# Optimization experiments

Measured on AMD Instinct MI355X. Metric: run time of the kernel, lower is better.

Reference implementation:

```python
import jax, jax.numpy as jnp
import numpy as np

B_, S_, D_ = 2, 1024, 768
EXPAND, HEADDIM, DSTATE = 2, 64, 64
DINNER = EXPAND * D_            # 1536
NHEADS = DINNER // HEADDIM      # 24
DMLP = int(2.5 * D_)            # 1920
PROJ = 2 * DINNER + 2 * NHEADS * DSTATE + NHEADS + NHEADS * (DSTATE // 2)  # 6936


def rms_norm(x, w, eps=1e-5):
    return x * jax.lax.rsqrt(jnp.mean(x * x, axis=-1, keepdims=True) + eps) * w


def apply_rope(x, angles):
    # x: (..., d_state), angles: (..., d_state//2)
    x1 = x[..., 0::2]
    x2 = x[..., 1::2]
    c, s = jnp.cos(angles), jnp.sin(angles)
    even = c * x1 - s * x2
    odd = s * x1 + c * x2
    return jnp.stack([even, odd], axis=-1).reshape(x.shape)


def ssm_scan(x, A, Bm, Cm):
    # x: (b,s,h,p), A: (b,s,h), Bm/Cm: (b,s,h,n)
    b, s, h, p = x.shape
    n = Bm.shape[-1]

    def step(hstate, inp):
        x_t, A_t, B_t, C_t = inp
        hstate = hstate * jnp.exp(A_t)[:, :, None, None] + jnp.einsum('bhn,bhp->bhpn', B_t, x_t)
        y_t = jnp.einsum('bhpn,bhn->bhp', hstate, C_t)
        return hstate, y_t

    h0 = jnp.zeros((b, h, p, n), dtype=x.dtype)
    xs = (jnp.swapaxes(x, 0, 1), jnp.swapaxes(A, 0, 1),
          jnp.swapaxes(Bm, 0, 1), jnp.swapaxes(Cm, 0, 1))
    _, ys = jax.lax.scan(step, h0, xs)
    return jnp.swapaxes(ys, 0, 1)  # (b,s,h,p)


def setup_inputs() -> dict:
    key = jax.random.key(0)
    ks = jax.random.split(key, 16)
    sc = 0.02
    return {
        'x': jax.random.normal(ks[0], (B_, S_, D_), dtype=jnp.float32),
        'norm1_w': jnp.ones((D_,), jnp.float32),
        'norm2_w': jnp.ones((D_,), jnp.float32),
        'in_proj_w': jax.random.normal(ks[1], (PROJ, D_), jnp.float32) * sc,
        'out_proj_w': jax.random.normal(ks[2], (D_, DINNER), jnp.float32) * sc,
        'A_log': jax.random.uniform(ks[3], (NHEADS,), jnp.float32, -4.0, -1.0),
        'D': jnp.ones((NHEADS,), jnp.float32),
        'dt_bias': jax.random.uniform(ks[4], (NHEADS,), jnp.float32, 0.001, 0.1),
        'B_bias': jnp.ones((1, NHEADS, DSTATE), jnp.float32),
        'C_bias': jnp.ones((1, NHEADS, DSTATE), jnp.float32),
        'Bnorm_w': jnp.ones((DSTATE,), jnp.float32),
        'Cnorm_w': jnp.ones((DSTATE,), jnp.float32),
        'mlp_gate_w': jax.random.normal(ks[5], (DMLP, D_), jnp.float32) * sc,
        'mlp_up_w': jax.random.normal(ks[6], (DMLP, D_), jnp.float32) * sc,
        'mlp_down_w': jax.random.normal(ks[7], (D_, DMLP), jnp.float32) * sc,
    }


def reference(x, norm1_w, norm2_w, in_proj_w, out_proj_w, A_log, D, dt_bias,
              B_bias, C_bias, Bnorm_w, Cnorm_w, mlp_gate_w, mlp_up_w, mlp_down_w):
    b, s, _ = x.shape
    h = rms_norm(x, norm1_w)
    proj = jnp.einsum('bsd,od->bso', h, in_proj_w)
    i = 0
    z = proj[..., i:i + DINNER]; i += DINNER
    x_ssm = proj[..., i:i + DINNER]; i += DINNER
    Bm = proj[..., i:i + NHEADS * DSTATE].reshape(b, s, NHEADS, DSTATE); i += NHEADS * DSTATE
    Cm = proj[..., i:i + NHEADS * DSTATE].reshape(b, s, NHEADS, DSTATE); i += NHEADS * DSTATE
    dt = proj[..., i:i + NHEADS]; i += NHEADS
    theta = proj[..., i:].reshape(b, s, NHEADS, DSTATE // 2)

    dt = jax.nn.softplus(dt + dt_bias)                 # (b,s,h)
    A = -jnp.exp(A_log) * dt                           # (b,s,h)
    alpha = jnp.exp(A)
    gamma = (alpha - 1.0) / (A + 1e-6) * 0.5 + 1.0

    Bm = rms_norm(Bm, Bnorm_w) + B_bias
    Cm = rms_norm(Cm, Cnorm_w) + C_bias
    cum_theta = jnp.cumsum(dt[..., None] * theta, axis=1)
    Bm = apply_rope(Bm, cum_theta)
    Cm = apply_rope(Cm, cum_theta)

    x_ssm = x_ssm.reshape(b, s, NHEADS, HEADDIM)
    x_scaled = x_ssm * gamma[..., None]
    y = ssm_scan(x_scaled, A, Bm, Cm)                  # (b,s,h,p)
    skip = (D[None, None, :] * x_ssm.sum(-1))[..., None]  # (b,s,h,1)
    y = (y + skip).reshape(b, s, DINNER)
    y = y * (z * jax.nn.sigmoid(z))
    y = jnp.einsum('bsi,oi->bso', y, out_proj_w)
    x = x + y
    h2 = rms_norm(x, norm2_w)
    g = jnp.einsum('bsd,od->bso', h2, mlp_gate_w)
    u = jnp.einsum('bsd,od->bso', h2, mlp_up_w)
    mlp = jnp.einsum('bsi,oi->bso', (g * jax.nn.sigmoid(g)) * u, mlp_down_w)
    return x + mlp
```

## Files before the change

### kernel.cpp

```cpp
#include <hip/hip_runtime.h>

typedef unsigned short u16;
typedef __attribute__((ext_vector_type(8))) short short8;
typedef __attribute__((ext_vector_type(4))) float f32x4;

constexpr int B_N    = 2;
constexpr int SEQ    = 1024;
constexpr int DMODEL = 768;
constexpr int DINNER = 1536;
constexpr int NH     = 24;
constexpr int DMLP   = 1920;
constexpr int NPROJ  = 6936;
constexpr int PP     = 7040;
constexpr int MROWS  = B_N * SEQ;
constexpr int NCHUNK = 16;
constexpr int CLEN   = 64;

__device__ __forceinline__ u16 f2bf(float f) {
  union { float f; unsigned u; } x; x.f = f;
  unsigned r = x.u + 0x7fffu + ((x.u >> 16) & 1u);
  return (u16)(r >> 16);
}
__device__ __forceinline__ float bf2f(u16 b) {
  union { unsigned u; float f; } x; x.u = ((unsigned)b) << 16; return x.f;
}

__device__ __forceinline__ void gld_lds16(const u16* g, u16* l) {
  __builtin_amdgcn_global_load_lds((const __attribute__((address_space(1))) void*)g,
                                   (__attribute__((address_space(3))) void*)l, 16, 0, 0);
}

__device__ __forceinline__ short8 frag(const u16* base, int row, int cb) {
  return *(const short8*)(base + row * 64 + ((cb ^ (row & 7)) << 3));
}
__device__ __forceinline__ int swz_idx(int row, int e) {
  return (((e >> 3) ^ (row & 7)) << 3) | (e & 7);
}

constexpr size_t E0  = (size_t)PP * DMODEL;
constexpr size_t E0s = (size_t)NPROJ * DMODEL;
constexpr size_t E1  = (size_t)DMODEL * DINNER;
constexpr size_t E2  = (size_t)DMLP * DMODEL;
constexpr size_t ETOT = E0 + E1 + 3 * E2;

__global__ void cast_all_kernel(const float* __restrict__ w_in, const float* __restrict__ w_out,
                                const float* __restrict__ w_g, const float* __restrict__ w_u,
                                const float* __restrict__ w_d,
                                u16* __restrict__ wb_in, u16* __restrict__ wb_out,
                                u16* __restrict__ wb_gu, u16* __restrict__ wb_d) {
  size_t i = ((size_t)blockIdx.x * 256 + threadIdx.x) * 4;
  if (i >= ETOT) return;
  float4 v; u16* dst;
  if (i < E0) {
    dst = wb_in + i;
    if (i < E0s) v = *(const float4*)(w_in + i);
    else { v.x = v.y = v.z = v.w = 0.f; }
  } else if (i < E0 + E1) {
    size_t k = i - E0; dst = wb_out + k; v = *(const float4*)(w_out + k);
  } else if (i < E0 + E1 + 2 * E2) {
    size_t k = i - E0 - E1;
    size_t r = k / DMODEL, col = k - r * DMODEL;
    const float* src = (r & 1) ? w_u : w_g;
    v = *(const float4*)(src + (r >> 1) * DMODEL + col);
    dst = wb_gu + k;
  } else {
    size_t k = i - E0 - E1 - 2 * E2; dst = wb_d + k; v = *(const float4*)(w_d + k);
  }
  short4 o;
  o.x = (short)f2bf(v.x); o.y = (short)f2bf(v.y);
  o.z = (short)f2bf(v.z); o.w = (short)f2bf(v.w);
  *(short4*)dst = o;
}

__global__ __launch_bounds__(256) void add_rmsnorm_kernel(
    const float* __restrict__ a, const float* __restrict__ b,
    const float* __restrict__ w, float* __restrict__ sum_out,
    u16* __restrict__ hout) {
  int row = blockIdx.x;
  int t = threadIdx.x;
  const float* pa = a + (size_t)row * DMODEL;
  const float* pb = b ? b + (size_t)row * DMODEL : nullptr;
  float v[3]; float ss = 0.f;
#pragma unroll
  for (int i = 0; i < 3; ++i) {
    int c = t + i * 256;
    float x = pa[c];
    if (pb) x += pb[c];
    v[i] = x; ss += x * x;
  }
#pragma unroll
  for (int o = 32; o > 0; o >>= 1) ss += __shfl_xor(ss, o);
  __shared__ float red[4];
  if ((t & 63) == 0) red[t >> 6] = ss;
  __syncthreads();
  ss = red[0] + red[1] + red[2] + red[3];
  float sc = rsqrtf(ss * (1.f / DMODEL) + 1e-5f);
#pragma unroll
  for (int i = 0; i < 3; ++i) {
    int c = t + i * 256;
    if (sum_out) sum_out[(size_t)row * DMODEL + c] = v[i];
    hout[(size_t)row * DMODEL + c] = f2bf(v[i] * sc * w[c]);
  }
}

template<int BM, int BN, int MODE>
__global__ __launch_bounds__(256) void gemm_bt_kernel(
    const u16* __restrict__ A, const u16* __restrict__ Bw,
    void* __restrict__ Cv, int K, int ldc, const float* __restrict__ addsrc) {
  constexpr int MI = BM / 32;
  constexpr int NJ = BN / 32;
  __shared__ u16 As[BM * 64];
  __shared__ u16 Bs[BN * 64];
  const int t = threadIdx.x;
  const int lane = t & 63;
  const int wave = t >> 6;
  const int wm = wave >> 1, wn = wave & 1;
  const int gx = gridDim.x, gy = gridDim.y;
  const int o = blockIdx.y * gx + blockIdx.x;
  const int nwg = gx * gy;
  const int cid = (o & 7) * (nwg >> 3) + (o >> 3);
  const int bx = cid / gy, by = cid - bx * gy;
  const int m0 = by * BM, n0 = bx * BN;
  f32x4 acc[MI][NJ] = {};
  const int rr = t >> 3;
  const int kc = (t & 7) * 8;
  const u16* ga = A + (size_t)(m0 + rr) * K + kc;
  const u16* gb = Bw + (size_t)(n0 + rr) * K + kc;
  for (int kt = 0; kt < K; kt += 64) {
    __syncthreads();
#pragma unroll
    for (int i = 0; i < MI; ++i)
      gld_lds16(ga + (size_t)i * 32 * K + kt, As + i * 2048 + t * 8);
#pragma unroll
    for (int i = 0; i < NJ; ++i)
      gld_lds16(gb + (size_t)i * 32 * K + kt, Bs + i * 2048 + t * 8);
    __syncthreads();
#pragma unroll
    for (int kh = 0; kh < 2; ++kh) {
      short8 af[MI], bfr[NJ];
#pragma unroll
      for (int i = 0; i < MI; ++i)
        af[i] = *(const short8*)(As + (wm * (BM / 2) + i * 16 + (lane & 15)) * 64 + kh * 32 + (lane >> 4) * 8);
#pragma unroll
      for (int j = 0; j < NJ; ++j)
        bfr[j] = *(const short8*)(Bs + (wn * (BN / 2) + j * 16 + (lane & 15)) * 64 + kh * 32 + (lane >> 4) * 8);
#pragma unroll
      for (int i = 0; i < MI; ++i)
#pragma unroll
        for (int j = 0; j < NJ; ++j)
          acc[i][j] = __builtin_amdgcn_mfma_f32_16x16x32_bf16(af[i], bfr[j], acc[i][j], 0, 0, 0);
    }
  }
  const int cr = (lane >> 4) * 4;
  const int cc = lane & 15;
#pragma unroll
  for (int i = 0; i < MI; ++i) {
#pragma unroll
    for (int j = 0; j < NJ; ++j) {
      int row = m0 + wm * (BM / 2) + i * 16 + cr;
      int col = n0 + wn * (BN / 2) + j * 16 + cc;
      if (MODE == 0) {
        float* C = (float*)Cv;
        float* cp = C + (size_t)row * ldc + col;
        if (addsrc) {
          const float* ap = addsrc + (size_t)row * ldc + col;
#pragma unroll
          for (int r = 0; r < 4; ++r) cp[(size_t)r * ldc] = acc[i][j][r] + ap[(size_t)r * ldc];
        } else {
#pragma unroll
          for (int r = 0; r < 4; ++r) cp[(size_t)r * ldc] = acc[i][j][r];
        }
      } else if (MODE == 1) {
        u16* C = (u16*)Cv;
#pragma unroll
        for (int r = 0; r < 4; ++r)
          C[(size_t)(row + r) * ldc + col] = f2bf(acc[i][j][r]);
      } else {
        u16* C = (u16*)Cv;
#pragma unroll
        for (int r = 0; r < 4; ++r) {
          float v = acc[i][j][r];
          float p = __shfl_xor(v, 1);
          if ((lane & 1) == 0) {
            float g = v, u = p;
            float res = g / (1.f + __expf(-g)) * u;
            C[(size_t)(row + r) * ldc + (col >> 1)] = f2bf(res);
          }
        }
      }
    }
  }
}

__global__ __launch_bounds__(256) void prep_kernel(
    u16* __restrict__ proj, const float* __restrict__ A_log,
    const float* __restrict__ Dv, const float* __restrict__ dt_bias,
    const float* __restrict__ B_bias, const float* __restrict__ C_bias,
    const float* __restrict__ Bnw, const float* __restrict__ Cnw,
    float* __restrict__ Abuf, float* __restrict__ skip_b,
    float* __restrict__ dtheta) {
  int wid = blockIdx.x * 4 + (threadIdx.x >> 6);
  int lane = threadIdx.x & 63;
  int m = wid / NH, h = wid - m * NH;
  u16* row = proj + (size_t)m * PP;

  float Braw = bf2f(row[3072 + h * 64 + lane]);
  float Craw = bf2f(row[4608 + h * 64 + lane]);
  float sb = Braw * Braw, sc2 = Craw * Craw;
#pragma unroll
  for (int o = 32; o > 0; o >>= 1) { sb += __shfl_xor(sb, o); sc2 += __shfl_xor(sc2, o); }
  float rb = rsqrtf(sb * (1.f / 64.f) + 1e-5f);
  float rc = rsqrtf(sc2 * (1.f / 64.f) + 1e-5f);
  row[3072 + h * 64 + lane] = f2bf(Braw * rb * Bnw[lane] + B_bias[h * 64 + lane]);
  row[4608 + h * 64 + lane] = f2bf(Craw * rc * Cnw[lane] + C_bias[h * 64 + lane]);

  float dtr = bf2f(row[6144 + h]) + dt_bias[h];
  float dt = dtr > 20.f ? dtr : log1pf(__expf(dtr));
  float A = -__expf(A_log[h]) * dt;
  float alpha = __expf(A);
  float gamma = (alpha - 1.f) / (A + 1e-6f) * 0.5f + 1.f;

  float xv = bf2f(row[1536 + h * 64 + lane]);
  float sx = xv;
#pragma unroll
  for (int o = 32; o > 0; o >>= 1) sx += __shfl_xor(sx, o);
  row[1536 + h * 64 + lane] = f2bf(xv * gamma);

  if (lane == 0) {
    Abuf[(size_t)m * NH + h] = A;
    skip_b[(size_t)m * NH + h] = Dv[h] * sx;
  }
  if (lane < 32) {
    float th = bf2f(row[6168 + h * 32 + lane]);
    dtheta[(size_t)m * 768 + h * 32 + lane] = dt * th;
  }
}

__global__ __launch_bounds__(256) void cumsum_a_kernel(float* __restrict__ dtheta,
                                                       float* __restrict__ ctot) {
  int bid = blockIdx.x;
  int cb = bid % 3, rest = bid / 3;
  int c = rest & 15, b = rest >> 4;
  int col = cb * 256 + threadIdx.x;
  float* p = dtheta + ((size_t)(b * SEQ + c * CLEN)) * 768 + col;
  float acc = 0.f;
#pragma unroll 4
  for (int s = 0; s < CLEN; ++s) {
    acc += p[(size_t)s * 768];
    p[(size_t)s * 768] = acc;
  }
  ctot[((size_t)b * NCHUNK + c) * 768 + col] = acc;
}

__global__ void cumsum_b_kernel(float* __restrict__ ctot) {
  int tid = blockIdx.x * 256 + threadIdx.x;
  int b = tid / 768, col = tid - b * 768;
  float pre = 0.f;
#pragma unroll
  for (int c = 0; c < NCHUNK; ++c) {
    size_t o = ((size_t)b * NCHUNK + c) * 768 + col;
    float v = ctot[o];
    ctot[o] = pre;
    pre += v;
  }
}

__global__ __launch_bounds__(256) void rope_kernel(
    u16* __restrict__ proj, const float* __restrict__ dtheta,
    const float* __restrict__ ctot) {
  int wid = blockIdx.x * 4 + (threadIdx.x >> 6);
  int lane = threadIdx.x & 63;
  int m = wid / NH, h = wid - m * NH;
  int j = lane & 31;
  int b = m >> 10;
  int c = (m >> 6) & 15;
  float ang = dtheta[(size_t)m * 768 + h * 32 + j] +
              ctot[((size_t)b * NCHUNK + c) * 768 + h * 32 + j];
  float sn, cs;
  __sincosf(ang, &sn, &cs);
  int base = (lane < 32) ? 3072 : 4608;
  unsigned* p = (unsigned*)(proj + (size_t)m * PP + base + h * 64) + j;
  unsigned v = *p;
  float x1 = bf2f((u16)(v & 0xffffu));
  float x2 = bf2f((u16)(v >> 16));
  *p = (unsigned)f2bf(cs * x1 - sn * x2) | ((unsigned)f2bf(sn * x1 + cs * x2) << 16);
}

__global__ __launch_bounds__(256) void houtA_kernel(
    const u16* __restrict__ proj, const float* __restrict__ Abuf,
    float* __restrict__ Lbuf, float* __restrict__ Hbuf) {
  int c = blockIdx.x & 15, bh = blockIdx.x >> 4;
  int b = bh / NH, h = bh - b * NH;
  int t = threadIdx.x, w = t >> 6, l = t & 63;
  __shared__ float sTmp[64][65];
  __shared__ u16 sBT[64 * 64];
  __shared__ u16 sXT[64 * 64];
  __shared__ float sRatio[64];
  int m0 = b * SEQ + c * CLEN;
  if (w == 0) {
    float v = Abuf[(size_t)(m0 + l) * NH + h];
#pragma unroll
    for (int o = 1; o < 64; o <<= 1) {
      float u = __shfl_up(v, o);
      if (l >= o) v += u;
    }
    Lbuf[(size_t)(m0 + l) * NH + h] = v;
    float L63 = __shfl(v, 63);
    sRatio[l] = __expf(L63 - v);
  }
  int rr = t >> 2, q = t & 3;
  {
    const u16* row = proj + (size_t)(m0 + rr) * PP + 3072 + h * 64;
#pragma unroll
    for (int k = 0; k < 4; ++k) {
      int e = q * 16 + k * 4;
      short4 sv = *(const short4*)(row + e);
      float4 ov;
      ov.x = bf2f((u16)sv.x); ov.y = bf2f((u16)sv.y);
      ov.z = bf2f((u16)sv.z); ov.w = bf2f((u16)sv.w);
      *(float4*)&sTmp[rr][e] = ov;
    }
  }
  __syncthreads();
  {
#pragma unroll
    for (int k = 0; k < 8; ++k) {
      int tw = (l + w * 8 + k) & 31;
      int t0 = tw * 2;
      unsigned pk = (unsigned)f2bf(sTmp[t0][l]) | ((unsigned)f2bf(sTmp[t0 + 1][l]) << 16);
      *(unsigned*)(sBT + l * 64 + swz_idx(l, t0)) = pk;
    }
  }
  __syncthreads();
  {
    const u16* row = proj + (size_t)(m0 + rr) * PP + 1536 + h * 64;
#pragma unroll
    for (int k = 0; k < 4; ++k) {
      int e = q * 16 + k * 4;
      short4 sv = *(const short4*)(row + e);
      float4 ov;
      ov.x = bf2f((u16)sv.x); ov.y = bf2f((u16)sv.y);
      ov.z = bf2f((u16)sv.z); ov.w = bf2f((u16)sv.w);
      *(float4*)&sTmp[rr][e] = ov;
    }
  }
  __syncthreads();
  {
#pragma unroll
    for (int k = 0; k < 8; ++k) {
      int tw = (l + w * 8 + k) & 31;
      int t0 = tw * 2;
      float v0 = sTmp[t0][l] * sRatio[t0];
      float v1 = sTmp[t0 + 1][l] * sRatio[t0 + 1];
      unsigned pk = (unsigned)f2bf(v0) | ((unsigned)f2bf(v1) << 16);
      *(unsigned*)(sXT + l * 64 + swz_idx(l, t0)) = pk;
    }
  }
  __syncthreads();
  f32x4 acc[4] = {};
#pragma unroll
  for (int kh = 0; kh < 2; ++kh) {
    int cb = kh * 4 + (l >> 4);
    short8 af = frag(sXT, w * 16 + (l & 15), cb);
#pragma unroll
    for (int j = 0; j < 4; ++j)
      acc[j] = __builtin_amdgcn_mfma_f32_16x16x32_bf16(af, frag(sBT, j * 16 + (l & 15), cb), acc[j], 0, 0, 0);
  }
  float* Hp = Hbuf + ((size_t)(bh * NCHUNK + c)) * 4096;
  int pr = w * 16 + ((l >> 4) << 2);
#pragma unroll
  for (int j = 0; j < 4; ++j)
#pragma unroll
    for (int r = 0; r < 4; ++r)
      Hp[(size_t)(pr + r) * 64 + j * 16 + (l & 15)] = acc[j][r];
}

__global__ __launch_bounds__(256) void scan2_kernel(
    float* __restrict__ Hbuf, const float* __restrict__ Lbuf) {
  int bh = blockIdx.x >> 4;
  int e = (blockIdx.x & 15) * 256 + threadIdx.x;
  int b = bh / NH, h = bh - b * NH;
  float S = 0.f;
  for (int c = 0; c < NCHUNK; ++c) {
    float* Hp = Hbuf + ((size_t)(bh * NCHUNK + c)) * 4096 + e;
    float P = __expf(Lbuf[(size_t)(b * SEQ + c * CLEN + CLEN - 1) * NH + h]);
    float v = *Hp;
    *Hp = S;
    S = P * S + v;
  }
}

__global__ __launch_bounds__(256) void intraB_kernel(
    const u16* __restrict__ proj, const float* __restrict__ Hbuf,
    const float* __restrict__ Lbuf, const float* __restrict__ skip_b,
    u16* __restrict__ actb) {
  int c = blockIdx.x & 15, bh = blockIdx.x >> 4;
  int b = bh / NH, h = bh - b * NH;
  int t = threadIdx.x, w = t >> 6, l = t & 63;
  __shared__ u16 sC[64 * 64];
  __shared__ u16 sBH[64 * 64];
  __shared__ u16 sXT[64 * 64];
  __shared__ union UU { float tmp[64][65]; u16 gm[64 * 64]; } uS;
  __shared__ float sL[64], sSkip[64];
  int m0 = b * SEQ + c * CLEN;
  if (w == 0) {
    sL[l] = Lbuf[(size_t)(m0 + l) * NH + h];
    sSkip[l] = skip_b[(size_t)(m0 + l) * NH + h];
  }
  int rr = t >> 2, q = t & 3;
  {
    const u16* rowC = proj + (size_t)(m0 + rr) * PP + 4608 + h * 64;
    const u16* rowB = proj + (size_t)(m0 + rr) * PP + 3072 + h * 64;
    const u16* rowX = proj + (size_t)(m0 + rr) * PP + 1536 + h * 64;
#pragma unroll
    for (int k = 0; k < 4; ++k) {
      int e = q * 16 + k * 4;
      int idx = swz_idx(rr, e);
      short4 cv = *(const short4*)(rowC + e);
      *(unsigned*)(sC + rr * 64 + idx)     = (unsigned)(u16)cv.x | ((unsigned)(u16)cv.y << 16);
      *(unsigned*)(sC + rr * 64 + idx + 2) = (unsigned)(u16)cv.z | ((unsigned)(u16)cv.w << 16);
      short4 bv = *(const short4*)(rowB + e);
      *(unsigned*)(sBH + rr * 64 + idx)     = (unsigned)(u16)bv.x | ((unsigned)(u16)bv.y << 16);
      *(unsigned*)(sBH + rr * 64 + idx + 2) = (unsigned)(u16)bv.z | ((unsigned)(u16)bv.w << 16);
      short4 xv = *(const short4*)(rowX + e);
      float4 ov;
      ov.x = bf2f((u16)xv.x); ov.y = bf2f((u16)xv.y);
      ov.z = bf2f((u16)xv.z); ov.w = bf2f((u16)xv.w);
      *(float4*)&uS.tmp[rr][e] = ov;
    }
  }
  __syncthreads();
  {
#pragma unroll
    for (int k = 0; k < 8; ++k) {
      int tw = (l + w * 8 + k) & 31;
      int t0 = tw * 2;
      unsigned pk = (unsigned)f2bf(uS.tmp[t0][l]) | ((unsigned)f2bf(uS.tmp[t0 + 1][l]) << 16);
      *(unsigned*)(sXT + l * 64 + swz_idx(l, t0)) = pk;
    }
  }
  __syncthreads();
  f32x4 g4[4] = {};
#pragma unroll
  for (int kh = 0; kh < 2; ++kh) {
    int cb = kh * 4 + (l >> 4);
    short8 af = frag(sC, w * 16 + (l & 15), cb);
#pragma unroll
    for (int j = 0; j < 4; ++j)
      g4[j] = __builtin_amdgcn_mfma_f32_16x16x32_bf16(af, frag(sBH, j * 16 + (l & 15), cb), g4[j], 0, 0, 0);
  }
  __syncthreads();
  {
    int sr = w * 16 + ((l >> 4) << 2);
#pragma unroll
    for (int j = 0; j < 4; ++j) {
      int tc = j * 16 + (l & 15);
#pragma unroll
      for (int r = 0; r < 4; ++r) {
        int s = sr + r;
        float gv = (tc <= s) ? g4[j][r] * __expf(sL[s] - sL[tc]) : 0.f;
        uS.gm[s * 64 + swz_idx(s, tc)] = f2bf(gv);
      }
    }
    const float* Hp = Hbuf + ((size_t)(bh * NCHUNK + c)) * 4096 + rr * 64;
#pragma unroll
    for (int k = 0; k < 4; ++k) {
      int e = q * 16 + k * 4;
      float4 v = *(const float4*)(Hp + e);
      unsigned lo = (unsigned)f2bf(v.x) | ((unsigned)f2bf(v.y) << 16);
      unsigned hi = (unsigned)f2bf(v.z) | ((unsigned)f2bf(v.w) << 16);
      int idx = swz_idx(rr, e);
      *(unsigned*)(sBH + rr * 64 + idx) = lo;
      *(unsigned*)(sBH + rr * 64 + idx + 2) = hi;
    }
  }
  __syncthreads();
  f32x4 y1[4] = {}, y2[4] = {};
#pragma unroll
  for (int kh = 0; kh < 2; ++kh) {
    int cb = kh * 4 + (l >> 4);
    short8 ag = frag(uS.gm, w * 16 + (l & 15), cb);
    short8 ac = frag(sC, w * 16 + (l & 15), cb);
#pragma unroll
    for (int j = 0; j < 4; ++j) {
      y1[j] = __builtin_amdgcn_mfma_f32_16x16x32_bf16(ag, frag(sXT, j * 16 + (l & 15), cb), y1[j], 0, 0, 0);
      y2[j] = __builtin_amdgcn_mfma_f32_16x16x32_bf16(ac, frag(sBH, j * 16 + (l & 15), cb), y2[j], 0, 0, 0);
    }
  }
  int sr = w * 16 + ((l >> 4) << 2);
#pragma unroll
  for (int r = 0; r < 4; ++r) {
    int s = sr + r;
    float scale = __expf(sL[s]);
    float skp = sSkip[s];
    size_t mrow = (size_t)(m0 + s);
#pragma unroll
    for (int j = 0; j < 4; ++j) {
      int p = j * 16 + (l & 15);
      float y = y1[j][r] + scale * y2[j][r] + skp;
      float z = bf2f(proj[mrow * PP + h * 64 + p]);
      float sg = 1.f / (1.f + __expf(-z));
      actb[mrow * DINNER + h * 64 + p] = f2bf(y * z * sg);
    }
  }
}

extern "C" void kernel_launch(void* const* d_in, const int* in_sizes, int n_in,
                              void* d_out, int out_size, void* d_ws, size_t ws_size,
                              hipStream_t stream) {
  (void)in_sizes; (void)n_in; (void)out_size; (void)ws_size;
  const float* x      = (const float*)d_in[0];
  const float* n1w    = (const float*)d_in[1];
  const float* n2w    = (const float*)d_in[2];
  const float* w_in   = (const float*)d_in[3];
  const float* w_out  = (const float*)d_in[4];
  const float* A_log  = (const float*)d_in[5];
  const float* Dv     = (const float*)d_in[6];
  const float* dt_b   = (const float*)d_in[7];
  const float* B_bias = (const float*)d_in[8];
  const float* C_bias = (const float*)d_in[9];
  const float* Bnw    = (const float*)d_in[10];
  const float* Cnw    = (const float*)d_in[11];
  const float* w_g    = (const float*)d_in[12];
  const float* w_u    = (const float*)d_in[13];
  const float* w_d    = (const float*)d_in[14];
  float* out = (float*)d_out;

  char* ws = (char*)d_ws;
  size_t off = 0;
  auto alloc = [&](size_t bytes) -> char* {
    char* p = ws + off;
    off = (off + bytes + 255) & ~(size_t)255;
    return p;
  };
  u16*   wb_in  = (u16*)  alloc(E0 * 2);
  u16*   wb_out = (u16*)  alloc(E1 * 2);
  u16*   wb_gu  = (u16*)  alloc(E2 * 2 * 2);
  u16*   wb_d   = (u16*)  alloc(E2 * 2);
  u16*   h1     = (u16*)  alloc((size_t)MROWS * DMODEL * 2);
  u16*   proj   = (u16*)  alloc((size_t)MROWS * PP * 2);
  float* Abuf   = (float*)alloc((size_t)MROWS * NH * 4);
  float* skip_b = (float*)alloc((size_t)MROWS * NH * 4);
  float* Lbuf   = (float*)alloc((size_t)MROWS * NH * 4);
  float* dtheta = (float*)alloc((size_t)MROWS * 768 * 4);
  float* ctot   = (float*)alloc((size_t)B_N * NCHUNK * 768 * 4);
  float* Hbuf   = (float*)alloc((size_t)B_N * NH * NCHUNK * 4096 * 4);
  u16*   actb   = (u16*)  alloc((size_t)MROWS * DINNER * 2);
  float* tmp1   = (float*)alloc((size_t)MROWS * DMODEL * 4);
  float* x2     = (float*)alloc((size_t)MROWS * DMODEL * 4);
  u16*   h2     = (u16*)  alloc((size_t)MROWS * DMODEL * 2);
  u16*   gub    = (u16*)  alloc((size_t)MROWS * DMLP * 2);

  cast_all_kernel<<<(int)((ETOT / 4 + 255) / 256), 256, 0, stream>>>(
      w_in, w_out, w_g, w_u, w_d, wb_in, wb_out, wb_gu, wb_d);
  add_rmsnorm_kernel<<<MROWS, 256, 0, stream>>>(x, nullptr, n1w, nullptr, h1);
  {
    dim3 g(PP / 128, MROWS / 64);
    gemm_bt_kernel<64, 128, 1><<<g, 256, 0, stream>>>(h1, wb_in, proj, DMODEL, PP, nullptr);
  }
  prep_kernel<<<MROWS * NH / 4, 256, 0, stream>>>(proj, A_log, Dv, dt_b, B_bias, C_bias,
                                                  Bnw, Cnw, Abuf, skip_b, dtheta);
  cumsum_a_kernel<<<B_N * NCHUNK * 3, 256, 0, stream>>>(dtheta, ctot);
  cumsum_b_kernel<<<6, 256, 0, stream>>>(ctot);
  rope_kernel<<<MROWS * NH / 4, 256, 0, stream>>>(proj, dtheta, ctot);
  houtA_kernel<<<B_N * NH * NCHUNK, 256, 0, stream>>>(proj, Abuf, Lbuf, Hbuf);
  scan2_kernel<<<B_N * NH * NCHUNK, 256, 0, stream>>>(Hbuf, Lbuf);
  intraB_kernel<<<B_N * NH * NCHUNK, 256, 0, stream>>>(proj, Hbuf, Lbuf, skip_b, actb);
  {
    dim3 g(DMODEL / 64, MROWS / 64);
    gemm_bt_kernel<64, 64, 0><<<g, 256, 0, stream>>>(actb, wb_out, tmp1, DINNER, DMODEL, nullptr);
  }
  add_rmsnorm_kernel<<<MROWS, 256, 0, stream>>>(x, tmp1, n2w, x2, h2);
  {
    dim3 g(2 * DMLP / 128, MROWS / 64);
    gemm_bt_kernel<64, 128, 2><<<g, 256, 0, stream>>>(h2, wb_gu, gub, DMODEL, DMLP, nullptr);
  }
  {
    dim3 g(DMODEL / 64, MROWS / 64);
    gemm_bt_kernel<64, 64, 0><<<g, 256, 0, stream>>>(gub, wb_d, out, DMLP, DMODEL, x2);
  }
}
```

Measured before the change: 295.3 us.

## Swizzle GEMM LDS tiles and move intra-chunk SSM output into first scan kernel

```diff
diff --git a/kernel.cpp b/kernel.cpp
--- a/kernel.cpp
+++ b/kernel.cpp
@@ -123,7 +123,7 @@
   const int m0 = by * BM, n0 = bx * BN;
   f32x4 acc[MI][NJ] = {};
   const int rr = t >> 3;
-  const int kc = (t & 7) * 8;
+  const int kc = (((t & 7) ^ (rr & 7))) * 8;
   const u16* ga = A + (size_t)(m0 + rr) * K + kc;
   const u16* gb = Bw + (size_t)(n0 + rr) * K + kc;
   for (int kt = 0; kt < K; kt += 64) {
@@ -137,13 +137,14 @@
     __syncthreads();
 #pragma unroll
     for (int kh = 0; kh < 2; ++kh) {
+      const int cq = kh * 4 + (lane >> 4);
       short8 af[MI], bfr[NJ];
 #pragma unroll
       for (int i = 0; i < MI; ++i)
-        af[i] = *(const short8*)(As + (wm * (BM / 2) + i * 16 + (lane & 15)) * 64 + kh * 32 + (lane >> 4) * 8);
+        af[i] = frag(As, wm * (BM / 2) + i * 16 + (lane & 15), cq);
 #pragma unroll
       for (int j = 0; j < NJ; ++j)
-        bfr[j] = *(const short8*)(Bs + (wn * (BN / 2) + j * 16 + (lane & 15)) * 64 + kh * 32 + (lane >> 4) * 8);
+        bfr[j] = frag(Bs, wn * (BN / 2) + j * 16 + (lane & 15), cq);
 #pragma unroll
       for (int i = 0; i < MI; ++i)
 #pragma unroll
@@ -286,16 +287,18 @@
   *p = (unsigned)f2bf(cs * x1 - sn * x2) | ((unsigned)f2bf(sn * x1 + cs * x2) << 16);
 }
 
-__global__ __launch_bounds__(256) void houtA_kernel(
+__global__ __launch_bounds__(256) void scanA_kernel(
     const u16* __restrict__ proj, const float* __restrict__ Abuf,
-    float* __restrict__ Lbuf, float* __restrict__ Hbuf) {
+    float* __restrict__ Lbuf, float* __restrict__ Hbuf,
+    float* __restrict__ y1b) {
   int c = blockIdx.x & 15, bh = blockIdx.x >> 4;
   int b = bh / NH, h = bh - b * NH;
   int t = threadIdx.x, w = t >> 6, l = t & 63;
   __shared__ float sTmp[64][65];
   __shared__ u16 sBT[64 * 64];
   __shared__ u16 sXT[64 * 64];
-  __shared__ float sRatio[64];
+  __shared__ u16 sGm[64 * 64];
+  __shared__ float sRatio[64], sL[64];
   int m0 = b * SEQ + c * CLEN;
   if (w == 0) {
     float v = Abuf[(size_t)(m0 + l) * NH + h];
@@ -305,6 +308,7 @@
       if (l >= o) v += u;
     }
     Lbuf[(size_t)(m0 + l) * NH + h] = v;
+    sL[l] = v;
     float L63 = __shfl(v, 63);
     sRatio[l] = __expf(L63 - v);
   }
@@ -321,13 +325,32 @@
       *(float4*)&sTmp[rr][e] = ov;
     }
   }
+  const u16* baseC = proj + (size_t)m0 * PP + 4608 + h * 64;
+  const u16* baseB = proj + (size_t)m0 * PP + 3072 + h * 64;
+  short8 cf[2], bgf[2][4];
+#pragma unroll
+  for (int kh = 0; kh < 2; ++kh) {
+    int cq = kh * 4 + (l >> 4);
+    cf[kh] = *(const short8*)(baseC + (size_t)(w * 16 + (l & 15)) * PP + cq * 8);
+#pragma unroll
+    for (int j = 0; j < 4; ++j)
+      bgf[kh][j] = *(const short8*)(baseB + (size_t)(j * 16 + (l & 15)) * PP + cq * 8);
+  }
   __syncthreads();
+  f32x4 g4[4] = {};
+#pragma unroll
+  for (int kh = 0; kh < 2; ++kh)
+#pragma unroll
+    for (int j = 0; j < 4; ++j)
+      g4[j] = __builtin_amdgcn_mfma_f32_16x16x32_bf16(cf[kh], bgf[kh][j], g4[j], 0, 0, 0);
   {
 #pragma unroll
     for (int k = 0; k < 8; ++k) {
       int tw = (l + w * 8 + k) & 31;
       int t0 = tw * 2;
-      unsigned pk = (unsigned)f2bf(sTmp[t0][l]) | ((unsigned)f2bf(sTmp[t0 + 1][l]) << 16);
+      float v0 = sTmp[t0][l] * sRatio[t0];
+      float v1 = sTmp[t0 + 1][l] * sRatio[t0 + 1];
+      unsigned pk = (unsigned)f2bf(v0) | ((unsigned)f2bf(v1) << 16);
       *(unsigned*)(sBT + l * 64 + swz_idx(l, t0)) = pk;
     }
   }
@@ -350,21 +373,35 @@
     for (int k = 0; k < 8; ++k) {
       int tw = (l + w * 8 + k) & 31;
       int t0 = tw * 2;
-      float v0 = sTmp[t0][l] * sRatio[t0];
-      float v1 = sTmp[t0 + 1][l] * sRatio[t0 + 1];
-      unsigned pk = (unsigned)f2bf(v0) | ((unsigned)f2bf(v1) << 16);
+      unsigned pk = (unsigned)f2bf(sTmp[t0][l]) | ((unsigned)f2bf(sTmp[t0 + 1][l]) << 16);
       *(unsigned*)(sXT + l * 64 + swz_idx(l, t0)) = pk;
     }
   }
+  {
+    int sr = w * 16 + ((l >> 4) << 2);
+#pragma unroll
+    for (int j = 0; j < 4; ++j) {
+      int tc = j * 16 + (l & 15);
+#pragma unroll
+      for (int r = 0; r < 4; ++r) {
+        int s = sr + r;
+        float gv = (tc <= s) ? g4[j][r] * __expf(sL[s] - sL[tc]) : 0.f;
+        sGm[s * 64 + swz_idx(s, tc)] = f2bf(gv);
+      }
+    }
+  }
   __syncthreads();
-  f32x4 acc[4] = {};
+  f32x4 y1[4] = {}, ho[4] = {};
 #pragma unroll
   for (int kh = 0; kh < 2; ++kh) {
-    int cb = kh * 4 + (l >> 4);
-    short8 af = frag(sXT, w * 16 + (l & 15), cb);
-#pragma unroll
-    for (int j = 0; j < 4; ++j)
-      acc[j] = __builtin_amdgcn_mfma_f32_16x16x32_bf16(af, frag(sBT, j * 16 + (l & 15), cb), acc[j], 0, 0, 0);
+    int cq = kh * 4 + (l >> 4);
+    short8 agm = frag(sGm, w * 16 + (l & 15), cq);
+    short8 axt = frag(sXT, w * 16 + (l & 15), cq);
+#pragma unroll
+    for (int j = 0; j < 4; ++j) {
+      y1[j] = __builtin_amdgcn_mfma_f32_16x16x32_bf16(agm, frag(sXT, j * 16 + (l & 15), cq), y1[j], 0, 0, 0);
+      ho[j] = __builtin_amdgcn_mfma_f32_16x16x32_bf16(axt, frag(sBT, j * 16 + (l & 15), cq), ho[j], 0, 0, 0);
+    }
   }
   float* Hp = Hbuf + ((size_t)(bh * NCHUNK + c)) * 4096;
   int pr = w * 16 + ((l >> 4) << 2);
@@ -372,7 +409,14 @@
   for (int j = 0; j < 4; ++j)
 #pragma unroll
     for (int r = 0; r < 4; ++r)
-      Hp[(size_t)(pr + r) * 64 + j * 16 + (l & 15)] = acc[j][r];
+      Hp[(size_t)(pr + r) * 64 + j * 16 + (l & 15)] = ho[j][r];
+#pragma unroll
+  for (int r = 0; r < 4; ++r) {
+    int s = pr + r;
+#pragma unroll
+    for (int j = 0; j < 4; ++j)
+      y1b[(size_t)(m0 + s) * DINNER + h * 64 + j * 16 + (l & 15)] = y1[j][r];
+  }
 }
 
 __global__ __launch_bounds__(256) void scan2_kernel(
@@ -390,103 +434,46 @@
   }
 }
 
-__global__ __launch_bounds__(256) void intraB_kernel(
+__global__ __launch_bounds__(256) void scanB_kernel(
     const u16* __restrict__ proj, const float* __restrict__ Hbuf,
     const float* __restrict__ Lbuf, const float* __restrict__ skip_b,
-    u16* __restrict__ actb) {
+    const float* __restrict__ y1b, u16* __restrict__ actb) {
   int c = blockIdx.x & 15, bh = blockIdx.x >> 4;
   int b = bh / NH, h = bh - b * NH;
   int t = threadIdx.x, w = t >> 6, l = t & 63;
-  __shared__ u16 sC[64 * 64];
-  __shared__ u16 sBH[64 * 64];
-  __shared__ u16 sXT[64 * 64];
-  __shared__ union UU { float tmp[64][65]; u16 gm[64 * 64]; } uS;
   __shared__ float sL[64], sSkip[64];
   int m0 = b * SEQ + c * CLEN;
   if (w == 0) {
     sL[l] = Lbuf[(size_t)(m0 + l) * NH + h];
     sSkip[l] = skip_b[(size_t)(m0 + l) * NH + h];
   }
-  int rr = t >> 2, q = t & 3;
-  {
-    const u16* rowC = proj + (size_t)(m0 + rr) * PP + 4608 + h * 64;
-    const u16* rowB = proj + (size_t)(m0 + rr) * PP + 3072 + h * 64;
-    const u16* rowX = proj + (size_t)(m0 + rr) * PP + 1536 + h * 64;
-#pragma unroll
-    for (int k = 0; k < 4; ++k) {
-      int e = q * 16 + k * 4;
-      int idx = swz_idx(rr, e);
-      short4 cv = *(const short4*)(rowC + e);
-      *(unsigned*)(sC + rr * 64 + idx)     = (unsigned)(u16)cv.x | ((unsigned)(u16)cv.y << 16);
-      *(unsigned*)(sC + rr * 64 + idx + 2) = (unsigned)(u16)cv.z | ((unsigned)(u16)cv.w << 16);
-      short4 bv = *(const short4*)(rowB + e);
-      *(unsigned*)(sBH + rr * 64 + idx)     = (unsigned)(u16)bv.x | ((unsigned)(u16)bv.y << 16);
-      *(unsigned*)(sBH + rr * 64 + idx + 2) = (unsigned)(u16)bv.z | ((unsigned)(u16)bv.w << 16);
-      short4 xv = *(const short4*)(rowX + e);
-      float4 ov;
-      ov.x = bf2f((u16)xv.x); ov.y = bf2f((u16)xv.y);
-      ov.z = bf2f((u16)xv.z); ov.w = bf2f((u16)xv.w);
-      *(float4*)&uS.tmp[rr][e] = ov;
+  const u16* baseC = proj + (size_t)m0 * PP + 4608 + h * 64;
+  const float* Hp = Hbuf + ((size_t)(bh * NCHUNK + c)) * 4096;
+  short8 cf[2], hf[2][4];
+#pragma unroll
+  for (int kh = 0; kh < 2; ++kh) {
+    int cq = kh * 4 + (l >> 4);
+    cf[kh] = *(const short8*)(baseC + (size_t)(w * 16 + (l & 15)) * PP + cq * 8);
+#pragma unroll
+    for (int j = 0; j < 4; ++j) {
+      const float* hp = Hp + (size_t)(j * 16 + (l & 15)) * 64 + cq * 8;
+      float4 a = *(const float4*)hp;
+      float4 b2 = *(const float4*)(hp + 4);
+      short8 hv;
+      hv[0] = (short)f2bf(a.x);  hv[1] = (short)f2bf(a.y);
+      hv[2] = (short)f2bf(a.z);  hv[3] = (short)f2bf(a.w);
+      hv[4] = (short)f2bf(b2.x); hv[5] = (short)f2bf(b2.y);
+      hv[6] = (short)f2bf(b2.z); hv[7] = (short)f2bf(b2.w);
+      hf[kh][j] = hv;
     }
   }
   __syncthreads();
-  {
-#pragma unroll
-    for (int k = 0; k < 8; ++k) {
-      int tw = (l + w * 8 + k) & 31;
-      int t0 = tw * 2;
-      unsigned pk = (unsigned)f2bf(uS.tmp[t0][l]) | ((unsigned)f2bf(uS.tmp[t0 + 1][l]) << 16);
-      *(unsigned*)(sXT + l * 64 + swz_idx(l, t0)) = pk;
-    }
-  }
-  __syncthreads();
-  f32x4 g4[4] = {};
-#pragma unroll
-  for (int kh = 0; kh < 2; ++kh) {
-    int cb = kh * 4 + (l >> 4);
-    short8 af = frag(sC, w * 16 + (l & 15), cb);
+  f32x4 y2[4] = {};
+#pragma unroll
+  for (int kh = 0; kh < 2; ++kh)
 #pragma unroll
     for (int j = 0; j < 4; ++j)
-      g4[j] = __builtin_amdgcn_mfma_f32_16x16x32_bf16(af, frag(sBH, j * 16 + (l & 15), cb), g4[j], 0, 0, 0);
-  }
-  __syncthreads();
-  {
-    int sr = w * 16 + ((l >> 4) << 2);
-#pragma unroll
-    for (int j = 0; j < 4; ++j) {
-      int tc = j * 16 + (l & 15);
-#pragma unroll
-      for (int r = 0; r < 4; ++r) {
-        int s = sr + r;
-        float gv = (tc <= s) ? g4[j][r] * __expf(sL[s] - sL[tc]) : 0.f;
-        uS.gm[s * 64 + swz_idx(s, tc)] = f2bf(gv);
-      }
-    }
-    const float* Hp = Hbuf + ((size_t)(bh * NCHUNK + c)) * 4096 + rr * 64;
-#pragma unroll
-    for (int k = 0; k < 4; ++k) {
-      int e = q * 16 + k * 4;
-      float4 v = *(const float4*)(Hp + e);
-      unsigned lo = (unsigned)f2bf(v.x) | ((unsigned)f2bf(v.y) << 16);
-      unsigned hi = (unsigned)f2bf(v.z) | ((unsigned)f2bf(v.w) << 16);
-      int idx = swz_idx(rr, e);
-      *(unsigned*)(sBH + rr * 64 + idx) = lo;
-      *(unsigned*)(sBH + rr * 64 + idx + 2) = hi;
-    }
-  }
-  __syncthreads();
-  f32x4 y1[4] = {}, y2[4] = {};
-#pragma unroll
-  for (int kh = 0; kh < 2; ++kh) {
-    int cb = kh * 4 + (l >> 4);
-    short8 ag = frag(uS.gm, w * 16 + (l & 15), cb);
-    short8 ac = frag(sC, w * 16 + (l & 15), cb);
-#pragma unroll
-    for (int j = 0; j < 4; ++j) {
-      y1[j] = __builtin_amdgcn_mfma_f32_16x16x32_bf16(ag, frag(sXT, j * 16 + (l & 15), cb), y1[j], 0, 0, 0);
-      y2[j] = __builtin_amdgcn_mfma_f32_16x16x32_bf16(ac, frag(sBH, j * 16 + (l & 15), cb), y2[j], 0, 0, 0);
-    }
-  }
+      y2[j] = __builtin_amdgcn_mfma_f32_16x16x32_bf16(cf[kh], hf[kh][j], y2[j], 0, 0, 0);
   int sr = w * 16 + ((l >> 4) << 2);
 #pragma unroll
   for (int r = 0; r < 4; ++r) {
@@ -497,7 +484,7 @@
 #pragma unroll
     for (int j = 0; j < 4; ++j) {
       int p = j * 16 + (l & 15);
-      float y = y1[j][r] + scale * y2[j][r] + skp;
+      float y = y1b[mrow * DINNER + h * 64 + p] + scale * y2[j][r] + skp;
       float z = bf2f(proj[mrow * PP + h * 64 + p]);
       float sg = 1.f / (1.f + __expf(-z));
       actb[mrow * DINNER + h * 64 + p] = f2bf(y * z * sg);
@@ -545,6 +532,7 @@
   float* dtheta = (float*)alloc((size_t)MROWS * 768 * 4);
   float* ctot   = (float*)alloc((size_t)B_N * NCHUNK * 768 * 4);
   float* Hbuf   = (float*)alloc((size_t)B_N * NH * NCHUNK * 4096 * 4);
+  float* y1b    = (float*)alloc((size_t)MROWS * DINNER * 4);
   u16*   actb   = (u16*)  alloc((size_t)MROWS * DINNER * 2);
   float* tmp1   = (float*)alloc((size_t)MROWS * DMODEL * 4);
   float* x2     = (float*)alloc((size_t)MROWS * DMODEL * 4);
@@ -563,9 +551,9 @@
   cumsum_a_kernel<<<B_N * NCHUNK * 3, 256, 0, stream>>>(dtheta, ctot);
   cumsum_b_kernel<<<6, 256, 0, stream>>>(ctot);
   rope_kernel<<<MROWS * NH / 4, 256, 0, stream>>>(proj, dtheta, ctot);
-  houtA_kernel<<<B_N * NH * NCHUNK, 256, 0, stream>>>(proj, Abuf, Lbuf, Hbuf);
+  scanA_kernel<<<B_N * NH * NCHUNK, 256, 0, stream>>>(proj, Abuf, Lbuf, Hbuf, y1b);
   scan2_kernel<<<B_N * NH * NCHUNK, 256, 0, stream>>>(Hbuf, Lbuf);
-  intraB_kernel<<<B_N * NH * NCHUNK, 256, 0, stream>>>(proj, Hbuf, Lbuf, skip_b, actb);
+  scanB_kernel<<<B_N * NH * NCHUNK, 256, 0, stream>>>(proj, Hbuf, Lbuf, skip_b, y1b, actb);
   {
     dim3 g(DMODEL / 64, MROWS / 64);
     gemm_bt_kernel<64, 64, 0><<<g, 256, 0, stream>>>(actb, wb_out, tmp1, DINNER, DMODEL, nullptr);
```

Result: faster. 283.0 us (-4.1%).
